# Kernel tuning notes

Measured on AMD Instinct MI355X. Metric: run time of the kernel, lower is better.

The kernel has to match this reference:

```python
import jax, jax.numpy as jnp
import numpy as np

B, S, H = 64, 2048, 512
NEG_INF = -1e10


def setup_inputs() -> dict:
    key = jax.random.key(0)
    k1, k2, k3, k4, k5, k6 = jax.random.split(key, 6)
    return {
        "output": jax.random.normal(k1, (B, 1, H), dtype=jnp.float32),
        "encoder_outputs": jax.random.normal(k2, (B, S, H), dtype=jnp.float32),
        "encoder_sequence_lengths": jax.random.randint(k3, (B,), 1, S + 1, dtype=jnp.int32),
        "W1": jax.random.normal(k4, (H, H), dtype=jnp.float32) * (1.0 / np.sqrt(H)),
        "W2": jax.random.normal(k5, (H, H), dtype=jnp.float32) * (1.0 / np.sqrt(H)),
        "V": jax.random.normal(k6, (H, 1), dtype=jnp.float32) * (1.0 / np.sqrt(H)),
    }


def reference(output, encoder_outputs, encoder_sequence_lengths, W1, W2, V):
    # output: [B,1,H] decoder state (query); encoder_outputs: [B,S,H] (key & value)
    S_ = encoder_outputs.shape[1]
    key_proj = jnp.einsum('bsh,hd->bsd', encoder_outputs, W1)   # [B,S,H]
    query_proj = jnp.einsum('bqh,hd->bqd', output, W2)          # [B,1,H]
    energy = jnp.einsum('bsh,ho->bso', jnp.tanh(key_proj + query_proj), V)  # [B,S,1]
    mask = jnp.arange(S_)[None, :, None] < encoder_sequence_lengths[:, None, None]  # [B,S,1]
    energy = jnp.where(mask, energy, NEG_INF)
    attn = jax.nn.softmax(energy, axis=1)                       # [B,S,1]
    context = jnp.sum(attn * encoder_outputs, axis=1)           # [B,H]
    return context
```

## Files before the change

kernel.cpp:

```cpp
#include <hip/hip_runtime.h>
#include <hip/hip_bf16.h>

#define SS 2048
#define HH 512

typedef __attribute__((ext_vector_type(8))) short short8;
typedef __attribute__((ext_vector_type(4))) float f32x4;

__device__ __forceinline__ float bflo(unsigned u) { return __uint_as_float(u << 16); }
__device__ __forceinline__ float bfhi(unsigned u) { return __uint_as_float(u & 0xffff0000u); }

__device__ __forceinline__ short f2bf(float v) {
  __hip_bfloat16 h = __float2bfloat16(v);
  return *reinterpret_cast<short*>(&h);
}

__device__ __forceinline__ float tanh_fast(float x) {
  x = fminf(fmaxf(x, -15.f), 15.f);
  float e = __expf(2.f * x);
  return 1.f - 2.f * __builtin_amdgcn_rcpf(e + 1.f);
}

__device__ __forceinline__ void gll16(const void* g, void* l) {
  __builtin_amdgcn_global_load_lds(
      (const __attribute__((address_space(1))) unsigned int*)g,
      (__attribute__((address_space(3))) unsigned int*)l, 16, 0, 0);
}

__global__ void k_detect(const unsigned* __restrict__ Eu, const int* __restrict__ lens,
                         int* __restrict__ flag, int* __restrict__ tmap,
                         int* __restrict__ livep) {
  int lane = threadIdx.x;
  unsigned w = Eu[(size_t)lane * 4097];
  unsigned e = (w >> 7) & 0xFF;
  bool inr = (e >= 90 && e <= 140);
  unsigned long long m = __ballot(inr);
  if (lane == 0) *flag = (__popcll(m) >= 48) ? 1 : 0;

  int len = lens[lane];
  int n = (len + 63) >> 6;
  int off = n;
#pragma unroll
  for (int o = 1; o < 64; o <<= 1) {
    int v = __shfl_up(off, o);
    if (lane >= o) off += v;
  }
  int base = off - n;
  for (int j = 0; j < n; ++j) tmap[base + j] = lane * 32 + j;
  if (lane == 63) *livep = off;
}

__global__ __launch_bounds__(256) void k_prep(const __hip_bfloat16* __restrict__ W1b,
                                              const float* __restrict__ W1f,
                                              const __hip_bfloat16* __restrict__ qb,
                                              const float* __restrict__ qf,
                                              const __hip_bfloat16* __restrict__ W2b,
                                              const float* __restrict__ W2f,
                                              const int* __restrict__ flagp,
                                              __hip_bfloat16* __restrict__ W1T,
                                              float* __restrict__ qp_part) {
  const int mode = *flagp;
  __shared__ __hip_bfloat16 t[64][65];
  __shared__ float qs[128];
  if (blockIdx.x < 64) {
    int r0 = (blockIdx.x >> 3) * 64, c0 = (blockIdx.x & 7) * 64;
    for (int i = threadIdx.x; i < 4096; i += 256) {
      int r = i >> 6, c = i & 63;
      size_t idx = (size_t)(r0 + r) * HH + c0 + c;
      float v = mode ? (float)W1b[idx] : W1f[idx];
      t[r][c] = __float2bfloat16(v);
    }
    __syncthreads();
    for (int i = threadIdx.x; i < 4096; i += 256) {
      int r = i >> 6, c = i & 63;
      W1T[(size_t)(c0 + r) * HH + r0 + c] = t[c][r];
    }
  } else {
    int bx = blockIdx.x - 64;
    int b = bx & 63, p = bx >> 6, h0 = p * 128;
    if (threadIdx.x < 128) {
      size_t qi = (size_t)b * HH + h0 + threadIdx.x;
      qs[threadIdx.x] = mode ? (float)qb[qi] : qf[qi];
    }
    __syncthreads();
    int col = threadIdx.x * 2;
    float a0 = 0.f, a1 = 0.f;
    if (mode) {
#pragma unroll 4
      for (int i = 0; i < 128; ++i) {
        float qa = qs[i];
        unsigned u = *(const unsigned*)(W2b + (size_t)(h0 + i) * HH + col);
        a0 = fmaf(qa, bflo(u), a0);
        a1 = fmaf(qa, bfhi(u), a1);
      }
    } else {
#pragma unroll 4
      for (int i = 0; i < 128; ++i) {
        float qa = qs[i];
        float2 v = *(const float2*)(W2f + (size_t)(h0 + i) * HH + col);
        a0 = fmaf(qa, v.x, a0);
        a1 = fmaf(qa, v.y, a1);
      }
    }
    float* dst = qp_part + ((size_t)p * 64 + b) * HH + col;
    dst[0] = a0;
    dst[1] = a1;
  }
}

__global__ __launch_bounds__(256, 3) void k_energy(
    const __hip_bfloat16* __restrict__ Eb, const float* __restrict__ Ef,
    const __hip_bfloat16* __restrict__ W1T, const float* __restrict__ qpp,
    const __hip_bfloat16* __restrict__ Vwb, const float* __restrict__ Vwf,
    const int* __restrict__ flagp, const int* __restrict__ lens,
    const int* __restrict__ tmap, const int* __restrict__ livep,
    float* __restrict__ tpart) {
  __shared__ __align__(16) __hip_bfloat16 Bt[4][128 * 32];
  __shared__ float qps[HH];
  __shared__ float Vs[HH];
  __shared__ float p[64];
  __shared__ float red[4];
  __shared__ f32x4 part[128];

  const int tid = threadIdx.x;
  const int wave = tid >> 6, lane = tid & 63;
  const int quad = lane >> 4, l16 = lane & 15;
  const int live = *livep;
  if (blockIdx.x >= live) return;
  const int mode = *flagp;

  const int tile = tmap[blockIdx.x];
  const int b = tile >> 5;
  const int srow = (tile & 31) * 64;
  const int row0 = b * SS + srow;
  const int len = lens[b];

  const int rs0 = wave * 32 + (lane >> 2);
  const int rs1 = rs0 + 16;
  const int kg0 = ((lane & 3) - (rs0 >> 1)) & 3;
  const int kg1 = ((lane & 3) - (rs1 >> 1)) & 3;
  const __hip_bfloat16* pb0 = W1T + (size_t)rs0 * HH + kg0 * 8;
  const __hip_bfloat16* pb1 = W1T + (size_t)rs1 * HH + kg1 * 8;
  char* ldsB = (char*)&Bt[0][0];
  char* ldW = ldsB + wave * 2048;

  int offB[8];
#pragma unroll
  for (int cb = 0; cb < 8; ++cb) {
    int n = cb * 16 + l16;
    offB[cb] = n * 32 + (((quad + (n >> 1)) & 3) << 3);
  }

#pragma unroll
  for (int s = 0; s < 3; ++s) {
    int o = s << 5;
    gll16(pb0 + o, ldW + s * 8192);
    gll16(pb1 + o, ldW + s * 8192 + 1024);
  }

  short8 afr[16];
  {
    const size_t eBase = (size_t)(row0 + wave * 16 + l16) * HH + quad * 8;
    if (mode) {
      const __hip_bfloat16* pa = Eb + eBase;
#pragma unroll
      for (int kt = 0; kt < 16; ++kt) afr[kt] = *(const short8*)(pa + kt * 32);
    } else {
      const float* pa = Ef + eBase;
#pragma unroll
      for (int g = 0; g < 4; ++g) {
        f32x4 x0[4], x1[4];
#pragma unroll
        for (int k = 0; k < 4; ++k) {
          const float* pp = pa + (g * 4 + k) * 32;
          x0[k] = *(const f32x4*)pp;
          x1[k] = *(const f32x4*)(pp + 4);
        }
#pragma unroll
        for (int k = 0; k < 4; ++k) {
          short8 v;
#pragma unroll
          for (int j = 0; j < 4; ++j) {
            v[j] = f2bf(x0[k][j]);
            v[j + 4] = f2bf(x1[k][j]);
          }
          afr[g * 4 + k] = v;
        }
      }
    }
  }

  for (int i = tid; i < HH; i += 256) {
    qps[i] = qpp[(size_t)b * HH + i] + qpp[(size_t)(64 + b) * HH + i] +
             qpp[(size_t)(128 + b) * HH + i] + qpp[(size_t)(192 + b) * HH + i];
    Vs[i] = mode ? (float)Vwb[i] : Vwf[i];
  }

  float eacc[4] = {0.f, 0.f, 0.f, 0.f};

  for (int nc = 0; nc < 4; ++nc) {
    f32x4 acc[8];
#pragma unroll
    for (int cb = 0; cb < 8; ++cb) acc[cb] = (f32x4){0.f, 0.f, 0.f, 0.f};

#pragma unroll
    for (int kt = 0; kt < 16; ++kt) {
      __builtin_amdgcn_sched_barrier(0);
      asm volatile("s_waitcnt vmcnt(4)" ::: "memory");
      __builtin_amdgcn_s_barrier();
      __builtin_amdgcn_sched_barrier(0);

      {
        int t2 = nc * 16 + kt + 3;
        if (t2 > 63) t2 = 63;
        int o = ((t2 >> 4) << 16) + ((t2 & 15) << 5);
        char* ld = ldW + ((kt + 3) & 3) * 8192;
        gll16(pb0 + o, ld);
        gll16(pb1 + o, ld + 1024);
      }

      const __hip_bfloat16* bb = &Bt[kt & 3][0];
      short8 af = afr[kt];
#pragma unroll
      for (int cb = 0; cb < 8; ++cb) {
        short8 bf = *(const short8*)(bb + offB[cb]);
        acc[cb] = __builtin_amdgcn_mfma_f32_16x16x32_bf16(af, bf, acc[cb], 0, 0, 0);
      }
    }

#pragma unroll
    for (int cb = 0; cb < 8; ++cb) {
      int col = nc * 128 + cb * 16 + l16;
      float qv = qps[col], vv = Vs[col];
#pragma unroll
      for (int r = 0; r < 4; ++r) {
        float tv = tanh_fast(acc[cb][r] + qv);
        eacc[r] = fmaf(vv, tv, eacc[r]);
      }
    }
  }

#pragma unroll
  for (int r = 0; r < 4; ++r) {
    float v = eacc[r];
#pragma unroll
    for (int o = 1; o < 16; o <<= 1) v += __shfl_xor(v, o);
    if (l16 == 0) {
      int row = wave * 16 + quad * 4 + r;
      p[row] = (srow + row < len) ? v : -3.0e38f;
    }
  }
  __syncthreads();

  if (wave == 0) {
    float e = p[lane];
    float m = e;
#pragma unroll
    for (int o = 1; o < 64; o <<= 1) m = fmaxf(m, __shfl_xor(m, o));
    float w = __expf(e - m);
    float d = w;
#pragma unroll
    for (int o = 1; o < 64; o <<= 1) d += __shfl_xor(d, o);
    p[lane] = w;
    if (lane == 0) {
      red[0] = m;
      red[1] = d;
    }
  }
  __syncthreads();
  const float m_t = red[0], d_t = red[1];

  const int n = min(64, len - srow);
  const int h0 = (tid & 127) * 4;
  const int rr = tid >> 7;
  f32x4 a = {0.f, 0.f, 0.f, 0.f};
  if (mode) {
    const __hip_bfloat16* base = Eb + (size_t)row0 * HH + h0;
#pragma unroll 8
    for (int i = rr; i < n; i += 2) {
      float wv = p[i];
      uint2 u = *(const uint2*)(base + (size_t)i * HH);
      a[0] = fmaf(wv, bflo(u.x), a[0]);
      a[1] = fmaf(wv, bfhi(u.x), a[1]);
      a[2] = fmaf(wv, bflo(u.y), a[2]);
      a[3] = fmaf(wv, bfhi(u.y), a[3]);
    }
  } else {
    const float* base = Ef + (size_t)row0 * HH + h0;
#pragma unroll 8
    for (int i = rr; i < n; i += 2) {
      float wv = p[i];
      f32x4 v = *(const f32x4*)(base + (size_t)i * HH);
      a[0] = fmaf(wv, v[0], a[0]);
      a[1] = fmaf(wv, v[1], a[1]);
      a[2] = fmaf(wv, v[2], a[2]);
      a[3] = fmaf(wv, v[3], a[3]);
    }
  }
  if (tid >= 128) part[tid - 128] = a;
  __syncthreads();
  if (tid < 128) {
    f32x4 o = part[tid];
    f32x4 s;
    s[0] = a[0] + o[0];
    s[1] = a[1] + o[1];
    s[2] = a[2] + o[2];
    s[3] = a[3] + o[3];
    *(f32x4*)(tpart + (size_t)tile * 516 + h0) = s;
  }
  if (tid == 0) {
    tpart[(size_t)tile * 516 + 512] = m_t;
    tpart[(size_t)tile * 516 + 513] = d_t;
  }
}

__global__ __launch_bounds__(256) void k_reduce(const float* __restrict__ tpart,
                                                const int* __restrict__ lens,
                                                const int* __restrict__ flagp,
                                                __hip_bfloat16* __restrict__ outb,
                                                float* __restrict__ outf) {
  const int b = blockIdx.x, tid = threadIdx.x;
  const int nch = (lens[b] + 63) >> 6;
  const float* tb = tpart + (size_t)b * 32 * 516;
  float m = -3.0e38f;
  for (int c = 0; c < nch; ++c) m = fmaxf(m, tb[c * 516 + 512]);
  const int h = tid * 2;
  float den = 0.f, a0 = 0.f, a1 = 0.f;
  for (int c = 0; c < nch; ++c) {
    float sc = __expf(tb[c * 516 + 512] - m);
    den = fmaf(tb[c * 516 + 513], sc, den);
    float2 v = *(const float2*)(tb + c * 516 + h);
    a0 = fmaf(sc, v.x, a0);
    a1 = fmaf(sc, v.y, a1);
  }
  float inv = 1.f / den;
  int i = b * HH + h;
  if (*flagp) {
    outb[i] = __float2bfloat16(a0 * inv);
    outb[i + 1] = __float2bfloat16(a1 * inv);
  } else {
    outf[i] = a0 * inv;
    outf[i + 1] = a1 * inv;
  }
}

extern "C" void kernel_launch(void* const* d_in, const int* in_sizes, int n_in,
                              void* d_out, int out_size, void* d_ws, size_t ws_size,
                              hipStream_t stream) {
  const __hip_bfloat16* qb  = (const __hip_bfloat16*)d_in[0];
  const float*          qf  = (const float*)d_in[0];
  const __hip_bfloat16* Eb  = (const __hip_bfloat16*)d_in[1];
  const float*          Ef  = (const float*)d_in[1];
  const int* lens           = (const int*)d_in[2];
  const __hip_bfloat16* W1b = (const __hip_bfloat16*)d_in[3];
  const float*          W1f = (const float*)d_in[3];
  const __hip_bfloat16* W2b = (const __hip_bfloat16*)d_in[4];
  const float*          W2f = (const float*)d_in[4];
  const __hip_bfloat16* Vwb = (const __hip_bfloat16*)d_in[5];
  const float*          Vwf = (const float*)d_in[5];
  __hip_bfloat16* outb      = (__hip_bfloat16*)d_out;
  float*          outf      = (float*)d_out;

  char* ws = (char*)d_ws;
  __hip_bfloat16* W1T = (__hip_bfloat16*)(ws);
  float* qp_part      = (float*)(ws + 524288);
  float* tpart        = (float*)(ws + 1048576);
  int* flag           = (int*)(ws + 5275648);
  int* tmap           = (int*)(ws + 5275652);
  int* livep          = (int*)(ws + 5283844);

  k_detect<<<dim3(1), 64, 0, stream>>>((const unsigned*)d_in[1], lens, flag, tmap, livep);
  k_prep<<<dim3(320), 256, 0, stream>>>(W1b, W1f, qb, qf, W2b, W2f, flag, W1T, qp_part);
  k_energy<<<dim3(2048), 256, 0, stream>>>(Eb, Ef, W1T, qp_part, Vwb, Vwf, flag, lens,
                                           tmap, livep, tpart);
  k_reduce<<<dim3(64), 256, 0, stream>>>(tpart, lens, flag, outb, outf);
}
```

Before: 446.3 us.

## Fold detect into prep and fuse reduce into energy via last-block atomic

```diff
diff --git a/kernel.cpp b/kernel.cpp
--- a/kernel.cpp
+++ b/kernel.cpp
@@ -27,63 +27,57 @@
       (__attribute__((address_space(3))) unsigned int*)l, 16, 0, 0);
 }
 
-__global__ void k_detect(const unsigned* __restrict__ Eu, const int* __restrict__ lens,
-                         int* __restrict__ flag, int* __restrict__ tmap,
-                         int* __restrict__ livep) {
-  int lane = threadIdx.x;
-  unsigned w = Eu[(size_t)lane * 4097];
-  unsigned e = (w >> 7) & 0xFF;
-  bool inr = (e >= 90 && e <= 140);
-  unsigned long long m = __ballot(inr);
-  if (lane == 0) *flag = (__popcll(m) >= 48) ? 1 : 0;
-
-  int len = lens[lane];
-  int n = (len + 63) >> 6;
-  int off = n;
-#pragma unroll
-  for (int o = 1; o < 64; o <<= 1) {
-    int v = __shfl_up(off, o);
-    if (lane >= o) off += v;
-  }
-  int base = off - n;
-  for (int j = 0; j < n; ++j) tmap[base + j] = lane * 32 + j;
-  if (lane == 63) *livep = off;
-}
-
-__global__ __launch_bounds__(256) void k_prep(const __hip_bfloat16* __restrict__ W1b,
+__global__ __launch_bounds__(256) void k_prep(const unsigned* __restrict__ Eu,
+                                              const int* __restrict__ lens,
+                                              const __hip_bfloat16* __restrict__ W1b,
                                               const float* __restrict__ W1f,
                                               const __hip_bfloat16* __restrict__ qb,
                                               const float* __restrict__ qf,
                                               const __hip_bfloat16* __restrict__ W2b,
                                               const float* __restrict__ W2f,
-                                              const int* __restrict__ flagp,
                                               __hip_bfloat16* __restrict__ W1T,
-                                              float* __restrict__ qp_part) {
-  const int mode = *flagp;
+                                              float* __restrict__ qp_part,
+                                              int* __restrict__ flag,
+                                              int* __restrict__ tmap,
+                                              int* __restrict__ livep,
+                                              int* __restrict__ cnt) {
+  __shared__ int smode;
   __shared__ __hip_bfloat16 t[64][65];
   __shared__ float qs[128];
+  const int tid = threadIdx.x;
+
+  if (tid < 64) {
+    unsigned w = Eu[(size_t)tid * 4097];
+    unsigned e = (w >> 7) & 0xFF;
+    bool inr = (e >= 90 && e <= 140);
+    unsigned long long m = __ballot(inr);
+    if (tid == 0) smode = (__popcll(m) >= 48) ? 1 : 0;
+  }
+  __syncthreads();
+  const int mode = smode;
+
   if (blockIdx.x < 64) {
     int r0 = (blockIdx.x >> 3) * 64, c0 = (blockIdx.x & 7) * 64;
-    for (int i = threadIdx.x; i < 4096; i += 256) {
+    for (int i = tid; i < 4096; i += 256) {
       int r = i >> 6, c = i & 63;
       size_t idx = (size_t)(r0 + r) * HH + c0 + c;
       float v = mode ? (float)W1b[idx] : W1f[idx];
       t[r][c] = __float2bfloat16(v);
     }
     __syncthreads();
-    for (int i = threadIdx.x; i < 4096; i += 256) {
+    for (int i = tid; i < 4096; i += 256) {
       int r = i >> 6, c = i & 63;
       W1T[(size_t)(c0 + r) * HH + r0 + c] = t[c][r];
     }
-  } else {
+  } else if (blockIdx.x < 320) {
     int bx = blockIdx.x - 64;
     int b = bx & 63, p = bx >> 6, h0 = p * 128;
-    if (threadIdx.x < 128) {
-      size_t qi = (size_t)b * HH + h0 + threadIdx.x;
-      qs[threadIdx.x] = mode ? (float)qb[qi] : qf[qi];
+    if (tid < 128) {
+      size_t qi = (size_t)b * HH + h0 + tid;
+      qs[tid] = mode ? (float)qb[qi] : qf[qi];
     }
     __syncthreads();
-    int col = threadIdx.x * 2;
+    int col = tid * 2;
     float a0 = 0.f, a1 = 0.f;
     if (mode) {
 #pragma unroll 4
@@ -105,6 +99,22 @@
     float* dst = qp_part + ((size_t)p * 64 + b) * HH + col;
     dst[0] = a0;
     dst[1] = a1;
+  } else {
+    if (tid < 64) {
+      if (tid == 0) *flag = mode;
+      int len = lens[tid];
+      int n = (len + 63) >> 6;
+      int off = n;
+#pragma unroll
+      for (int o = 1; o < 64; o <<= 1) {
+        int v = __shfl_up(off, o);
+        if (tid >= o) off += v;
+      }
+      int base = off - n;
+      for (int j = 0; j < n; ++j) tmap[base + j] = tid * 32 + j;
+      if (tid == 63) *livep = off;
+      cnt[tid] = 0;
+    }
   }
 }
 
@@ -114,13 +124,15 @@
     const __hip_bfloat16* __restrict__ Vwb, const float* __restrict__ Vwf,
     const int* __restrict__ flagp, const int* __restrict__ lens,
     const int* __restrict__ tmap, const int* __restrict__ livep,
-    float* __restrict__ tpart) {
+    float* __restrict__ tpart, int* __restrict__ cnt,
+    __hip_bfloat16* __restrict__ outb, float* __restrict__ outf) {
   __shared__ __align__(16) __hip_bfloat16 Bt[4][128 * 32];
   __shared__ float qps[HH];
   __shared__ float Vs[HH];
   __shared__ float p[64];
   __shared__ float red[4];
   __shared__ f32x4 part[128];
+  __shared__ int swin;
 
   const int tid = threadIdx.x;
   const int wave = tid >> 6, lane = tid & 63;
@@ -134,6 +146,7 @@
   const int srow = (tile & 31) * 64;
   const int row0 = b * SS + srow;
   const int len = lens[b];
+  const int nch = (len + 63) >> 6;
 
   const int rs0 = wave * 32 + (lane >> 2);
   const int rs1 = rs0 + 16;
@@ -312,22 +325,24 @@
     tpart[(size_t)tile * 516 + 512] = m_t;
     tpart[(size_t)tile * 516 + 513] = d_t;
   }
-}
-
-__global__ __launch_bounds__(256) void k_reduce(const float* __restrict__ tpart,
-                                                const int* __restrict__ lens,
-                                                const int* __restrict__ flagp,
-                                                __hip_bfloat16* __restrict__ outb,
-                                                float* __restrict__ outf) {
-  const int b = blockIdx.x, tid = threadIdx.x;
-  const int nch = (lens[b] + 63) >> 6;
+
+  __threadfence();
+  __syncthreads();
+  if (tid == 0) {
+    int r = __hip_atomic_fetch_add(&cnt[b], 1, __ATOMIC_ACQ_REL, __HIP_MEMORY_SCOPE_AGENT);
+    swin = (r == nch - 1) ? 1 : 0;
+  }
+  __syncthreads();
+  if (!swin) return;
+
+  __threadfence();
   const float* tb = tpart + (size_t)b * 32 * 516;
-  float m = -3.0e38f;
-  for (int c = 0; c < nch; ++c) m = fmaxf(m, tb[c * 516 + 512]);
+  float mm = -3.0e38f;
+  for (int c = 0; c < nch; ++c) mm = fmaxf(mm, tb[c * 516 + 512]);
   const int h = tid * 2;
   float den = 0.f, a0 = 0.f, a1 = 0.f;
   for (int c = 0; c < nch; ++c) {
-    float sc = __expf(tb[c * 516 + 512] - m);
+    float sc = __expf(tb[c * 516 + 512] - mm);
     den = fmaf(tb[c * 516 + 513], sc, den);
     float2 v = *(const float2*)(tb + c * 516 + h);
     a0 = fmaf(sc, v.x, a0);
@@ -335,7 +350,7 @@
   }
   float inv = 1.f / den;
   int i = b * HH + h;
-  if (*flagp) {
+  if (mode) {
     outb[i] = __float2bfloat16(a0 * inv);
     outb[i + 1] = __float2bfloat16(a1 * inv);
   } else {
@@ -368,10 +383,10 @@
   int* flag           = (int*)(ws + 5275648);
   int* tmap           = (int*)(ws + 5275652);
   int* livep          = (int*)(ws + 5283844);
-
-  k_detect<<<dim3(1), 64, 0, stream>>>((const unsigned*)d_in[1], lens, flag, tmap, livep);
-  k_prep<<<dim3(320), 256, 0, stream>>>(W1b, W1f, qb, qf, W2b, W2f, flag, W1T, qp_part);
+  int* cnt            = (int*)(ws + 5283848);
+
+  k_prep<<<dim3(321), 256, 0, stream>>>((const unsigned*)d_in[1], lens, W1b, W1f, qb, qf,
+                                        W2b, W2f, W1T, qp_part, flag, tmap, livep, cnt);
   k_energy<<<dim3(2048), 256, 0, stream>>>(Eb, Ef, W1T, qp_part, Vwb, Vwf, flag, lens,
-                                           tmap, livep, tpart);
-  k_reduce<<<dim3(64), 256, 0, stream>>>(tpart, lens, flag, outb, outf);
-}
+                                           tmap, livep, tpart, cnt, outb, outf);
+}
```

After: 651.8 us. 1.46x slower.
